# Kernel optimization log

Measured on AMD Instinct MI355X. Metric: run time of the kernel, lower is better.

Reference implementation:

```python
import jax, jax.numpy as jnp
import numpy as np

B = 8192
E = 1024  # embedding_size
P = 512   # projection_size
TEMPERATURE = 0.1
NEG_INF = -9e15
EPS = 1e-8


def setup_inputs() -> dict:
    key = jax.random.key(0)
    kx, kw, kb = jax.random.split(key, 3)
    x = jax.random.normal(kx, (B, 2 * E), dtype=jnp.float32)
    lim = 1.0 / np.sqrt(E)
    # torch nn.Linear default init: uniform(-1/sqrt(in), 1/sqrt(in))
    w = jax.random.uniform(kw, (E, P), jnp.float32, -lim, lim)
    b = jax.random.uniform(kb, (P,), jnp.float32, -lim, lim)
    return {"x": x, "w": w, "b": b}


def reference(x, w, b):
    e = x.shape[1] // 2
    # NOTE: source applies codon_projection to BOTH halves (aminoacid_projection unused)
    z_codon = jax.nn.relu(x[:, :e]) @ w + b          # [B, P]
    z_amino = jax.nn.relu(x[:, e:]) @ w + b          # [B, P]
    z = jnp.concatenate([z_codon, z_amino], axis=1)  # [B, 2P]

    # cosine similarity via normalize + GEMM instead of O(B^2*D) broadcast
    norm = jnp.maximum(jnp.linalg.norm(z, axis=-1, keepdims=True), EPS)
    zn = z / norm
    cos_sim = zn @ zn.T                              # [B, B]

    n = cos_sim.shape[0]
    idx = jnp.arange(n)
    # mask self-similarity BEFORE temperature division (matches source order)
    cos_sim = jnp.where(idx[:, None] == idx[None, :], NEG_INF, cos_sim)
    cos_sim = cos_sim / TEMPERATURE

    # pos_mask = eye rolled by B//2 along dim 0: pos[i] = cos_sim[i, (i - B//2) % B]
    pos = cos_sim[idx, (idx - n // 2) % n]
    nll = -pos + jax.nn.logsumexp(cos_sim, axis=-1)
    return nll.mean()
```

## Files before the change

kernel.cpp:

```cpp
#include <hip/hip_runtime.h>
#include <hip/hip_bf16.h>
#include <stdint.h>


typedef __attribute__((ext_vector_type(8))) __bf16 bf16x8;
typedef __attribute__((ext_vector_type(4))) float f32x4;
typedef __attribute__((ext_vector_type(4))) int i32x4;
typedef __attribute__((ext_vector_type(8))) int i32x8;

__device__ __forceinline__ unsigned short f2bf(float f) {
  union { float f; unsigned int u; } v; v.f = f;
  unsigned int u = v.u;
  u += 0x7FFFu + ((u >> 16) & 1u);
  return (unsigned short)(u >> 16);
}

__device__ __forceinline__ float bf2f(unsigned short s) {
  return __uint_as_float(((unsigned int)s) << 16);
}

__global__ __launch_bounds__(256) void prep2_kernel(
    const float* __restrict__ x, const float* __restrict__ w,
    unsigned char* __restrict__ x8, unsigned char* __restrict__ wt8,
    float* __restrict__ sumexp, float* __restrict__ out) {
  int tid = blockIdx.x * 256 + threadIdx.x;
  float4 v = ((const float4*)x)[tid];
  int p = __builtin_amdgcn_cvt_pk_fp8_f32(fmaxf(v.x, 0.f) * 16.f,
                                          fmaxf(v.y, 0.f) * 16.f, 0, false);
  p = __builtin_amdgcn_cvt_pk_fp8_f32(fmaxf(v.z, 0.f) * 16.f,
                                      fmaxf(v.w, 0.f) * 16.f, p, true);
  ((int*)x8)[tid] = p;
  if (tid < 512 * 1024) {
    int k = tid & 1023, n = tid >> 10;
    int q = __builtin_amdgcn_cvt_pk_fp8_f32(w[k * 512 + n] * 64.f, 0.f, 0, false);
    wt8[(n << 10) + k] = (unsigned char)(q & 0xFF);
  }
  if (tid < 8192) sumexp[tid] = 0.f;
  if (tid == 0) out[0] = 0.f;
}

__global__ __launch_bounds__(256) void gemm1q_kernel(
    const unsigned char* __restrict__ x8, const unsigned char* __restrict__ wt8,
    const float* __restrict__ bias, unsigned short* __restrict__ z) {
  __shared__ unsigned char As[16384] __attribute__((aligned(16)));
  __shared__ unsigned char Bs[16384] __attribute__((aligned(16)));
  int b = blockIdx.x;
  int kk = b >> 3;
  int i0 = ((b & 7) * 16 + (kk >> 2)) * 128;
  int n0 = (kk & 3) * 128;

  int tid = threadIdx.x, L = tid & 63, w = tid >> 6;
  int wm = w >> 1, wn = w & 1;
  int l4 = L & 15, q = L >> 4;
  int panel = q * 4096;

  int lp = L ^ ((L >> 3) & 7);
  int srow = w * 32 + (lp >> 1), sh = lp & 1;

  f32x4 acc[4][4];
#pragma unroll
  for (int a = 0; a < 4; ++a)
#pragma unroll
    for (int bq = 0; bq < 4; ++bq) acc[a][bq] = (f32x4)0.f;

  const unsigned char* Ag = x8 + (size_t)(i0 + srow) * 1024 + sh * 16;
  const unsigned char* Bg = wt8 + (size_t)(n0 + srow) * 1024 + sh * 16;

#pragma unroll 1
  for (int k0 = 0; k0 < 1024; k0 += 128) {
    __syncthreads();
#pragma unroll
    for (int t = 0; t < 4; ++t)
      __builtin_amdgcn_global_load_lds(
          (const __attribute__((address_space(1))) void*)(Ag + k0 + t * 32),
          (__attribute__((address_space(3))) void*)(As + t * 4096 + (tid & ~63) * 16),
          16, 0, 0);
#pragma unroll
    for (int t = 0; t < 4; ++t)
      __builtin_amdgcn_global_load_lds(
          (const __attribute__((address_space(1))) void*)(Bg + k0 + t * 32),
          (__attribute__((address_space(3))) void*)(Bs + t * 4096 + (tid & ~63) * 16),
          16, 0, 0);
    __syncthreads();
    i32x8 afr[4];
#pragma unroll
    for (int mt = 0; mt < 4; ++mt) {
      int row = wm * 64 + mt * 16 + l4;
      int p0 = (row * 2) ^ ((row >> 2) & 7);
      i32x4 lo = *(const i32x4*)(As + panel + p0 * 16);
      i32x4 hi = *(const i32x4*)(As + panel + (p0 ^ 1) * 16);
      afr[mt] = (i32x8){lo.x, lo.y, lo.z, lo.w, hi.x, hi.y, hi.z, hi.w};
    }
#pragma unroll
    for (int nt = 0; nt < 4; ++nt) {
      int row = wn * 64 + nt * 16 + l4;
      int p0 = (row * 2) ^ ((row >> 2) & 7);
      i32x4 lo = *(const i32x4*)(Bs + panel + p0 * 16);
      i32x4 hi = *(const i32x4*)(Bs + panel + (p0 ^ 1) * 16);
      i32x8 bfr = (i32x8){lo.x, lo.y, lo.z, lo.w, hi.x, hi.y, hi.z, hi.w};
#pragma unroll
      for (int mt = 0; mt < 4; ++mt)
        acc[mt][nt] = __builtin_amdgcn_mfma_scale_f32_16x16x128_f8f6f4(
            afr[mt], bfr, acc[mt][nt], 0, 0,
            0, 0x7F7F7F7F, 0, 0x7F7F7F7F);
    }
  }

  const float SC = 1.0f / 1024.0f;
#pragma unroll
  for (int nt = 0; nt < 4; ++nt) {
    int n = n0 + wn * 64 + nt * 16 + l4;
    float bn = bias[n];
#pragma unroll
    for (int mt = 0; mt < 4; ++mt) {
      int ib = i0 + wm * 64 + mt * 16 + q * 4;
#pragma unroll
      for (int r = 0; r < 4; ++r)
        z[(size_t)(ib + r) * 512 + n] = f2bf(acc[mt][nt][r] * SC + bn);
    }
  }
}

__global__ __launch_bounds__(256) void norm_kernel(
    const unsigned short* __restrict__ z, unsigned char* __restrict__ zn8) {
  int row = blockIdx.x, t = threadIdx.x;
  ushort4 u = ((const ushort4*)z)[row * 256 + t];
  float a0 = bf2f(u.x), a1 = bf2f(u.y), a2 = bf2f(u.z), a3 = bf2f(u.w);
  float ss = a0 * a0 + a1 * a1 + a2 * a2 + a3 * a3;
#pragma unroll
  for (int off = 1; off < 64; off <<= 1) ss += __shfl_xor(ss, off);
  __shared__ float red[4];
  if ((t & 63) == 0) red[t >> 6] = ss;
  __syncthreads();
  float tot = red[0] + red[1] + red[2] + red[3];
  float inv = 16.f / fmaxf(sqrtf(tot), 1e-8f);
  int p = __builtin_amdgcn_cvt_pk_fp8_f32(a0 * inv, a1 * inv, 0, false);
  p = __builtin_amdgcn_cvt_pk_fp8_f32(a2 * inv, a3 * inv, p, true);
  ((int*)zn8)[row * 256 + t] = p;
}

__global__ __launch_bounds__(256, 3) void gemm2_kernel(
    const unsigned char* __restrict__ zn8,
    float* __restrict__ sumexp, float* __restrict__ pos) {
  __shared__ unsigned char As[16384] __attribute__((aligned(16)));
  __shared__ unsigned char Bs[16384] __attribute__((aligned(16)));
  int g = (blockIdx.x & 7) * 260 + (blockIdx.x >> 3);
  int SI = 0, rem = g;
#pragma unroll 1
  for (SI = 0; SI < 8; ++SI) {
    int rowcnt = 36 + (7 - SI) * 64;
    if (rem < rowcnt) break;
    rem -= rowcnt;
  }
  int bi, bj;
  if (rem < 36) {
    int ti = 0;
    while (rem >= 8 - ti) { rem -= 8 - ti; ++ti; }
    bi = SI * 8 + ti;
    bj = bi + rem;
  } else {
    rem -= 36;
    int SJ = SI + 1 + (rem >> 6);
    int l = rem & 63;
    bi = SI * 8 + (l >> 3);
    bj = SJ * 8 + (l & 7);
  }
  bool diag = (bi == bj);
  int i0 = bi * 128, j0 = bj * 128;

  int tid = threadIdx.x, L = tid & 63, w = tid >> 6;
  int wm = w >> 1, wn = w & 1;
  int l4 = L & 15;
  int panel = (L >> 4) * 4096;

  int lp = L ^ ((L >> 3) & 7);
  int srow = w * 32 + (lp >> 1), sh = lp & 1;

  f32x4 acc[4][4];
#pragma unroll
  for (int a = 0; a < 4; ++a)
#pragma unroll
    for (int bq = 0; bq < 4; ++bq) acc[a][bq] = (f32x4)0.f;

  const unsigned char* Ag = zn8 + (i0 + srow) * 1024 + sh * 16;
  const unsigned char* Bg = zn8 + (j0 + srow) * 1024 + sh * 16;
  const unsigned char* Bsrc = diag ? (const unsigned char*)As : (const unsigned char*)Bs;

#pragma unroll 1
  for (int k0 = 0; k0 < 1024; k0 += 128) {
    __syncthreads();
#pragma unroll
    for (int t = 0; t < 4; ++t)
      __builtin_amdgcn_global_load_lds(
          (const __attribute__((address_space(1))) void*)(Ag + k0 + t * 32),
          (__attribute__((address_space(3))) void*)(As + t * 4096 + (tid & ~63) * 16),
          16, 0, 0);
    if (!diag) {
#pragma unroll
      for (int t = 0; t < 4; ++t)
        __builtin_amdgcn_global_load_lds(
            (const __attribute__((address_space(1))) void*)(Bg + k0 + t * 32),
            (__attribute__((address_space(3))) void*)(Bs + t * 4096 + (tid & ~63) * 16),
            16, 0, 0);
    }
    __syncthreads();
    i32x8 afr[4];
#pragma unroll
    for (int mt = 0; mt < 4; ++mt) {
      int row = wm * 64 + mt * 16 + l4;
      int p0 = (row * 2) ^ ((row >> 2) & 7);
      i32x4 lo = *(const i32x4*)(As + panel + p0 * 16);
      i32x4 hi = *(const i32x4*)(As + panel + (p0 ^ 1) * 16);
      afr[mt] = (i32x8){lo.x, lo.y, lo.z, lo.w, hi.x, hi.y, hi.z, hi.w};
    }
#pragma unroll
    for (int nt = 0; nt < 4; ++nt) {
      int row = wn * 64 + nt * 16 + l4;
      int p0 = (row * 2) ^ ((row >> 2) & 7);
      i32x4 lo = *(const i32x4*)(Bsrc + panel + p0 * 16);
      i32x4 hi = *(const i32x4*)(Bsrc + panel + (p0 ^ 1) * 16);
      i32x8 bfr = (i32x8){lo.x, lo.y, lo.z, lo.w, hi.x, hi.y, hi.z, hi.w};
#pragma unroll
      for (int mt = 0; mt < 4; ++mt)
        acc[mt][nt] = __builtin_amdgcn_mfma_scale_f32_16x16x128_f8f6f4(
            afr[mt], bfr, acc[mt][nt], 0, 0,
            0, 0x7F7F7F7F, 0, 0x7F7F7F7F);
    }
  }

  const float SC = 10.0f / 256.0f;
  float rs[4][4];
  float cs[4] = {0.f, 0.f, 0.f, 0.f};
#pragma unroll
  for (int mt = 0; mt < 4; ++mt)
#pragma unroll
    for (int r = 0; r < 4; ++r) rs[mt][r] = 0.f;
  int ib = i0 + wm * 64 + ((L >> 4) << 2);
  int jb = j0 + wn * 64 + l4;
#pragma unroll
  for (int mt = 0; mt < 4; ++mt)
#pragma unroll
    for (int nt = 0; nt < 4; ++nt) {
      int j = jb + nt * 16;
#pragma unroll
      for (int r = 0; r < 4; ++r) {
        int i = ib + mt * 16 + r;
        float s = acc[mt][nt][r] * SC;
        if (j == (i ^ 4096)) { pos[i] = s; pos[j] = s; }
        float e = (i == j) ? 0.f : __expf(s);
        rs[mt][r] += e;
        if (!diag) cs[nt] += e;
      }
    }
#pragma unroll
  for (int mt = 0; mt < 4; ++mt)
#pragma unroll
    for (int r = 0; r < 4; ++r) {
      float v = rs[mt][r];
      v += __shfl_xor(v, 1); v += __shfl_xor(v, 2);
      v += __shfl_xor(v, 4); v += __shfl_xor(v, 8);
      rs[mt][r] = v;
    }
  int sel = l4;
  float myv = rs[0][0];
#pragma unroll
  for (int mt = 0; mt < 4; ++mt)
#pragma unroll
    for (int r = 0; r < 4; ++r)
      if (sel == mt * 4 + r) myv = rs[mt][r];
  int rowi = i0 + wm * 64 + (sel >> 2) * 16 + ((L >> 4) << 2) + (sel & 3);
  atomicAdd(&sumexp[rowi], myv);
  if (!diag) {
#pragma unroll
    for (int nt = 0; nt < 4; ++nt) {
      float v = cs[nt];
      v += __shfl_xor(v, 16); v += __shfl_xor(v, 32);
      if ((L >> 4) == 0) atomicAdd(&sumexp[jb + nt * 16], v);
    }
  }
}

__global__ __launch_bounds__(512) void finalize_kernel(
    const float* __restrict__ sumexp, const float* __restrict__ pos,
    float* __restrict__ out) {
  int t = threadIdx.x;
  int i = blockIdx.x * 512 + t;
  float s = logf(sumexp[i]) - pos[i];
#pragma unroll
  for (int off = 1; off < 64; off <<= 1) s += __shfl_xor(s, off);
  __shared__ float red[8];
  if ((t & 63) == 0) red[t >> 6] = s;
  __syncthreads();
  if (t == 0) {
    float tot = 0.f;
    for (int k2 = 0; k2 < 8; ++k2) tot += red[k2];
    atomicAdd(out, tot * (1.0f / 8192.0f));
  }
}

extern "C" void kernel_launch(void* const* d_in, const int* in_sizes, int n_in,
                              void* d_out, int out_size, void* d_ws, size_t ws_size,
                              hipStream_t stream) {
  const float* x = (const float*)d_in[0];
  const float* w = (const float*)d_in[1];
  const float* b = (const float*)d_in[2];
  float* out = (float*)d_out;
  char* ws = (char*)d_ws;
  unsigned char* wt8 = (unsigned char*)(ws);
  unsigned char* x8  = (unsigned char*)(ws + 1048576);
  unsigned short* z  = (unsigned short*)(ws + 17825792);
  unsigned char* zn8 = (unsigned char*)(ws + 68157440);
  float* sumexp      = (float*)(ws + 84934656);
  float* pos         = (float*)(ws + 84967424);

  prep2_kernel<<<16384, 256, 0, stream>>>(x, w, x8, wt8, sumexp, out);
  gemm1q_kernel<<<512, 256, 0, stream>>>(x8, wt8, b, z);
  norm_kernel<<<8192, 256, 0, stream>>>(z, zn8);
  gemm2_kernel<<<2080, 256, 0, stream>>>(zn8, sumexp, pos);
  finalize_kernel<<<16, 512, 0, stream>>>(sumexp, pos, out);
}
```

Before: 175.4 us.

## Double-buffer LDS tiles in both FP8 GEMM kernels to overlap loads with MFMA

Both GEMM kernels now use a 64 KB shared buffer split into two stages for A and B. The next K-slice is issued with global_load_lds while the current slice is consumed by MFMAs, and there is one barrier per stage instead of two. The aim is to hide global-to-LDS latency behind compute. Doubling LDS cuts gemm2 occupancy from 3 to 2 blocks per CU via launch bounds, and overlap depends on the async load not being waited on early.

```diff
diff --git a/kernel.cpp b/kernel.cpp
--- a/kernel.cpp
+++ b/kernel.cpp
@@ -39,11 +39,10 @@
   if (tid == 0) out[0] = 0.f;
 }
 
-__global__ __launch_bounds__(256) void gemm1q_kernel(
+__global__ __launch_bounds__(256, 2) void gemm1q_kernel(
     const unsigned char* __restrict__ x8, const unsigned char* __restrict__ wt8,
     const float* __restrict__ bias, unsigned short* __restrict__ z) {
-  __shared__ unsigned char As[16384] __attribute__((aligned(16)));
-  __shared__ unsigned char Bs[16384] __attribute__((aligned(16)));
+  __shared__ unsigned char smem[65536] __attribute__((aligned(16)));
   int b = blockIdx.x;
   int kk = b >> 3;
   int i0 = ((b & 7) * 16 + (kk >> 2)) * 128;
@@ -56,6 +55,7 @@
 
   int lp = L ^ ((L >> 3) & 7);
   int srow = w * 32 + (lp >> 1), sh = lp & 1;
+  int ldst = (tid & ~63) * 16;
 
   f32x4 acc[4][4];
 #pragma unroll
@@ -66,37 +66,39 @@
   const unsigned char* Ag = x8 + (size_t)(i0 + srow) * 1024 + sh * 16;
   const unsigned char* Bg = wt8 + (size_t)(n0 + srow) * 1024 + sh * 16;
 
-#pragma unroll 1
-  for (int k0 = 0; k0 < 1024; k0 += 128) {
-    __syncthreads();
+  auto stage = [&](int buf, int k0) {
 #pragma unroll
     for (int t = 0; t < 4; ++t)
       __builtin_amdgcn_global_load_lds(
           (const __attribute__((address_space(1))) void*)(Ag + k0 + t * 32),
-          (__attribute__((address_space(3))) void*)(As + t * 4096 + (tid & ~63) * 16),
+          (__attribute__((address_space(3))) void*)(smem + buf * 16384 + t * 4096 + ldst),
           16, 0, 0);
 #pragma unroll
     for (int t = 0; t < 4; ++t)
       __builtin_amdgcn_global_load_lds(
           (const __attribute__((address_space(1))) void*)(Bg + k0 + t * 32),
-          (__attribute__((address_space(3))) void*)(Bs + t * 4096 + (tid & ~63) * 16),
+          (__attribute__((address_space(3))) void*)(smem + 32768 + buf * 16384 + t * 4096 + ldst),
           16, 0, 0);
-    __syncthreads();
+  };
+
+  auto compute = [&](int buf) {
+    const unsigned char* Asb = smem + buf * 16384;
+    const unsigned char* Bsb = smem + 32768 + buf * 16384;
     i32x8 afr[4];
 #pragma unroll
     for (int mt = 0; mt < 4; ++mt) {
       int row = wm * 64 + mt * 16 + l4;
       int p0 = (row * 2) ^ ((row >> 2) & 7);
-      i32x4 lo = *(const i32x4*)(As + panel + p0 * 16);
-      i32x4 hi = *(const i32x4*)(As + panel + (p0 ^ 1) * 16);
+      i32x4 lo = *(const i32x4*)(Asb + panel + p0 * 16);
+      i32x4 hi = *(const i32x4*)(Asb + panel + (p0 ^ 1) * 16);
       afr[mt] = (i32x8){lo.x, lo.y, lo.z, lo.w, hi.x, hi.y, hi.z, hi.w};
     }
 #pragma unroll
     for (int nt = 0; nt < 4; ++nt) {
       int row = wn * 64 + nt * 16 + l4;
       int p0 = (row * 2) ^ ((row >> 2) & 7);
-      i32x4 lo = *(const i32x4*)(Bs + panel + p0 * 16);
-      i32x4 hi = *(const i32x4*)(Bs + panel + (p0 ^ 1) * 16);
+      i32x4 lo = *(const i32x4*)(Bsb + panel + p0 * 16);
+      i32x4 hi = *(const i32x4*)(Bsb + panel + (p0 ^ 1) * 16);
       i32x8 bfr = (i32x8){lo.x, lo.y, lo.z, lo.w, hi.x, hi.y, hi.z, hi.w};
 #pragma unroll
       for (int mt = 0; mt < 4; ++mt)
@@ -104,6 +106,18 @@
             afr[mt], bfr, acc[mt][nt], 0, 0,
             0, 0x7F7F7F7F, 0, 0x7F7F7F7F);
     }
+  };
+
+  stage(0, 0);
+  __syncthreads();
+#pragma unroll 1
+  for (int k0 = 0; k0 < 1024; k0 += 256) {
+    stage(1, k0 + 128);
+    compute(0);
+    __syncthreads();
+    if (k0 < 768) stage(0, k0 + 256);
+    compute(1);
+    __syncthreads();
   }
 
   const float SC = 1.0f / 1024.0f;
@@ -139,11 +153,10 @@
   ((int*)zn8)[row * 256 + t] = p;
 }
 
-__global__ __launch_bounds__(256, 3) void gemm2_kernel(
+__global__ __launch_bounds__(256, 2) void gemm2_kernel(
     const unsigned char* __restrict__ zn8,
     float* __restrict__ sumexp, float* __restrict__ pos) {
-  __shared__ unsigned char As[16384] __attribute__((aligned(16)));
-  __shared__ unsigned char Bs[16384] __attribute__((aligned(16)));
+  __shared__ unsigned char smem[65536] __attribute__((aligned(16)));
   int g = (blockIdx.x & 7) * 260 + (blockIdx.x >> 3);
   int SI = 0, rem = g;
 #pragma unroll 1
@@ -175,6 +188,7 @@
 
   int lp = L ^ ((L >> 3) & 7);
   int srow = w * 32 + (lp >> 1), sh = lp & 1;
+  int ldst = (tid & ~63) * 16;
 
   f32x4 acc[4][4];
 #pragma unroll
@@ -184,41 +198,42 @@
 
   const unsigned char* Ag = zn8 + (i0 + srow) * 1024 + sh * 16;
   const unsigned char* Bg = zn8 + (j0 + srow) * 1024 + sh * 16;
-  const unsigned char* Bsrc = diag ? (const unsigned char*)As : (const unsigned char*)Bs;
-
-#pragma unroll 1
-  for (int k0 = 0; k0 < 1024; k0 += 128) {
-    __syncthreads();
+
+  auto stageA = [&](int buf, int k0) {
 #pragma unroll
     for (int t = 0; t < 4; ++t)
       __builtin_amdgcn_global_load_lds(
           (const __attribute__((address_space(1))) void*)(Ag + k0 + t * 32),
-          (__attribute__((address_space(3))) void*)(As + t * 4096 + (tid & ~63) * 16),
+          (__attribute__((address_space(3))) void*)(smem + buf * 16384 + t * 4096 + ldst),
           16, 0, 0);
-    if (!diag) {
-#pragma unroll
-      for (int t = 0; t < 4; ++t)
-        __builtin_amdgcn_global_load_lds(
-            (const __attribute__((address_space(1))) void*)(Bg + k0 + t * 32),
-            (__attribute__((address_space(3))) void*)(Bs + t * 4096 + (tid & ~63) * 16),
-            16, 0, 0);
-    }
-    __syncthreads();
+  };
+  auto stageB = [&](int buf, int k0) {
+#pragma unroll
+    for (int t = 0; t < 4; ++t)
+      __builtin_amdgcn_global_load_lds(
+          (const __attribute__((address_space(1))) void*)(Bg + k0 + t * 32),
+          (__attribute__((address_space(3))) void*)(smem + 32768 + buf * 16384 + t * 4096 + ldst),
+          16, 0, 0);
+  };
+
+  auto compute = [&](int buf) {
+    const unsigned char* Asb = smem + buf * 16384;
+    const unsigned char* Bsb = diag ? Asb : smem + 32768 + buf * 16384;
     i32x8 afr[4];
 #pragma unroll
     for (int mt = 0; mt < 4; ++mt) {
       int row = wm * 64 + mt * 16 + l4;
       int p0 = (row * 2) ^ ((row >> 2) & 7);
-      i32x4 lo = *(const i32x4*)(As + panel + p0 * 16);
-      i32x4 hi = *(const i32x4*)(As + panel + (p0 ^ 1) * 16);
+      i32x4 lo = *(const i32x4*)(Asb + panel + p0 * 16);
+      i32x4 hi = *(const i32x4*)(Asb + panel + (p0 ^ 1) * 16);
       afr[mt] = (i32x8){lo.x, lo.y, lo.z, lo.w, hi.x, hi.y, hi.z, hi.w};
     }
 #pragma unroll
     for (int nt = 0; nt < 4; ++nt) {
       int row = wn * 64 + nt * 16 + l4;
       int p0 = (row * 2) ^ ((row >> 2) & 7);
-      i32x4 lo = *(const i32x4*)(Bsrc + panel + p0 * 16);
-      i32x4 hi = *(const i32x4*)(Bsrc + panel + (p0 ^ 1) * 16);
+      i32x4 lo = *(const i32x4*)(Bsb + panel + p0 * 16);
+      i32x4 hi = *(const i32x4*)(Bsb + panel + (p0 ^ 1) * 16);
       i32x8 bfr = (i32x8){lo.x, lo.y, lo.z, lo.w, hi.x, hi.y, hi.z, hi.w};
 #pragma unroll
       for (int mt = 0; mt < 4; ++mt)
@@ -226,6 +241,23 @@
             afr[mt], bfr, acc[mt][nt], 0, 0,
             0, 0x7F7F7F7F, 0, 0x7F7F7F7F);
     }
+  };
+
+  stageA(0, 0);
+  if (!diag) stageB(0, 0);
+  __syncthreads();
+#pragma unroll 1
+  for (int k0 = 0; k0 < 1024; k0 += 256) {
+    stageA(1, k0 + 128);
+    if (!diag) stageB(1, k0 + 128);
+    compute(0);
+    __syncthreads();
+    if (k0 < 768) {
+      stageA(0, k0 + 256);
+      if (!diag) stageB(0, k0 + 256);
+    }
+    compute(1);
+    __syncthreads();
   }
 
   const float SC = 10.0f / 256.0f;
```

New measurement: 176.5 us. About the same (+0.6%).

## Enlarge gram GEMM tiles to 256x256 with double-buffered LDS and interleaved prefetch

Applied to the files above, without the earlier changes.

Reworks the symmetric fp8 gram GEMM from 128x128 tiles with 4 waves to 256x256 tiles with 8 waves over 528 upper-triangle blocks. K-chunks go into double-buffered 128KB LDS, and the next chunk's global-to-LDS loads are split into quarters interleaved between MFMA phases, with setprio and barriers in between. The aim is more operand reuse per byte loaded and hiding load latency behind compute. The cost is one block per CU because of the large LDS, many more barriers, and fewer blocks, which may leave load imbalance across CUs.

```diff
diff --git a/kernel.cpp b/kernel.cpp
--- a/kernel.cpp
+++ b/kernel.cpp
@@ -3,7 +3,6 @@
 #include <stdint.h>
 
 
-typedef __attribute__((ext_vector_type(8))) __bf16 bf16x8;
 typedef __attribute__((ext_vector_type(4))) float f32x4;
 typedef __attribute__((ext_vector_type(4))) int i32x4;
 typedef __attribute__((ext_vector_type(8))) int i32x8;
@@ -139,106 +138,169 @@
   ((int*)zn8)[row * 256 + t] = p;
 }
 
-__global__ __launch_bounds__(256, 3) void gemm2_kernel(
+__global__ __launch_bounds__(512) void gemm2_kernel(
     const unsigned char* __restrict__ zn8,
     float* __restrict__ sumexp, float* __restrict__ pos) {
-  __shared__ unsigned char As[16384] __attribute__((aligned(16)));
-  __shared__ unsigned char Bs[16384] __attribute__((aligned(16)));
-  int g = (blockIdx.x & 7) * 260 + (blockIdx.x >> 3);
-  int SI = 0, rem = g;
+  __shared__ unsigned char smem[131072] __attribute__((aligned(16)));
+  int g = (blockIdx.x & 7) * 66 + (blockIdx.x >> 3);
+  int rem = g, bi = 0;
 #pragma unroll 1
-  for (SI = 0; SI < 8; ++SI) {
-    int rowcnt = 36 + (7 - SI) * 64;
-    if (rem < rowcnt) break;
-    rem -= rowcnt;
-  }
-  int bi, bj;
-  if (rem < 36) {
-    int ti = 0;
-    while (rem >= 8 - ti) { rem -= 8 - ti; ++ti; }
-    bi = SI * 8 + ti;
-    bj = bi + rem;
-  } else {
-    rem -= 36;
-    int SJ = SI + 1 + (rem >> 6);
-    int l = rem & 63;
-    bi = SI * 8 + (l >> 3);
-    bj = SJ * 8 + (l & 7);
-  }
+  while (rem >= 32 - bi) { rem -= 32 - bi; ++bi; }
+  int bj = bi + rem;
   bool diag = (bi == bj);
-  int i0 = bi * 128, j0 = bj * 128;
+  int i0 = bi * 256, j0 = bj * 256;
 
   int tid = threadIdx.x, L = tid & 63, w = tid >> 6;
-  int wm = w >> 1, wn = w & 1;
-  int l4 = L & 15;
-  int panel = (L >> 4) * 4096;
+  int wm = w >> 2, wn = w & 3;
+  int l4 = L & 15, q = L >> 4;
+  int panel = q * 8192;
 
   int lp = L ^ ((L >> 3) & 7);
   int srow = w * 32 + (lp >> 1), sh = lp & 1;
-
-  f32x4 acc[4][4];
-#pragma unroll
-  for (int a = 0; a < 4; ++a)
+  int ldst = (tid & ~63) * 16;
+
+  int pA[8], pB[4];
+#pragma unroll
+  for (int mt = 0; mt < 8; ++mt) {
+    int r = wm * 128 + mt * 16 + l4;
+    pA[mt] = ((r * 2) ^ ((r >> 2) & 7)) * 16;
+  }
+#pragma unroll
+  for (int nt = 0; nt < 4; ++nt) {
+    int r = wn * 64 + nt * 16 + l4;
+    pB[nt] = ((r * 2) ^ ((r >> 2) & 7)) * 16;
+  }
+
+  f32x4 acc[8][4];
+#pragma unroll
+  for (int a = 0; a < 8; ++a)
 #pragma unroll
     for (int bq = 0; bq < 4; ++bq) acc[a][bq] = (f32x4)0.f;
 
-  const unsigned char* Ag = zn8 + (i0 + srow) * 1024 + sh * 16;
-  const unsigned char* Bg = zn8 + (j0 + srow) * 1024 + sh * 16;
-  const unsigned char* Bsrc = diag ? (const unsigned char*)As : (const unsigned char*)Bs;
+  const unsigned char* Ag = zn8 + (size_t)(i0 + srow) * 1024 + sh * 16;
+  const unsigned char* Bg = zn8 + (size_t)(j0 + srow) * 1024 + sh * 16;
+
+  auto stA = [&](int nc, int kk, int t) {
+    __builtin_amdgcn_global_load_lds(
+        (const __attribute__((address_space(1))) void*)(Ag + kk + t * 32),
+        (__attribute__((address_space(3))) void*)(smem + nc * 32768 + t * 8192 + ldst),
+        16, 0, 0);
+  };
+  auto stB = [&](int nc, int kk, int t) {
+    __builtin_amdgcn_global_load_lds(
+        (const __attribute__((address_space(1))) void*)(Bg + kk + t * 32),
+        (__attribute__((address_space(3))) void*)(smem + 65536 + nc * 32768 + t * 8192 + ldst),
+        16, 0, 0);
+  };
+
+  stA(0, 0, 0); stA(0, 0, 1); stA(0, 0, 2); stA(0, 0, 3);
+  if (!diag) { stB(0, 0, 0); stB(0, 0, 1); stB(0, 0, 2); stB(0, 0, 3); }
+  asm volatile("s_waitcnt vmcnt(0)" ::: "memory");
+  __builtin_amdgcn_s_barrier();
+  __builtin_amdgcn_sched_barrier(0);
 
 #pragma unroll 1
-  for (int k0 = 0; k0 < 1024; k0 += 128) {
-    __syncthreads();
-#pragma unroll
-    for (int t = 0; t < 4; ++t)
-      __builtin_amdgcn_global_load_lds(
-          (const __attribute__((address_space(1))) void*)(Ag + k0 + t * 32),
-          (__attribute__((address_space(3))) void*)(As + t * 4096 + (tid & ~63) * 16),
-          16, 0, 0);
-    if (!diag) {
-#pragma unroll
-      for (int t = 0; t < 4; ++t)
-        __builtin_amdgcn_global_load_lds(
-            (const __attribute__((address_space(1))) void*)(Bg + k0 + t * 32),
-            (__attribute__((address_space(3))) void*)(Bs + t * 4096 + (tid & ~63) * 16),
-            16, 0, 0);
-    }
-    __syncthreads();
-    i32x8 afr[4];
+  for (int t = 0; t < 8; ++t) {
+    int c = t & 1, nc = c ^ 1;
+    const unsigned char* Asb = smem + c * 32768;
+    const unsigned char* Bsb = diag ? Asb : smem + 65536 + c * 32768;
+    int k1 = t * 128 + 128;
+    bool st = (t < 7);
+
+    i32x8 afr[4], bf0[2], bf1[2];
 #pragma unroll
     for (int mt = 0; mt < 4; ++mt) {
-      int row = wm * 64 + mt * 16 + l4;
-      int p0 = (row * 2) ^ ((row >> 2) & 7);
-      i32x4 lo = *(const i32x4*)(As + panel + p0 * 16);
-      i32x4 hi = *(const i32x4*)(As + panel + (p0 ^ 1) * 16);
+      i32x4 lo = *(const i32x4*)(Asb + panel + pA[mt]);
+      i32x4 hi = *(const i32x4*)(Asb + panel + (pA[mt] ^ 16));
       afr[mt] = (i32x8){lo.x, lo.y, lo.z, lo.w, hi.x, hi.y, hi.z, hi.w};
     }
 #pragma unroll
-    for (int nt = 0; nt < 4; ++nt) {
-      int row = wn * 64 + nt * 16 + l4;
-      int p0 = (row * 2) ^ ((row >> 2) & 7);
-      i32x4 lo = *(const i32x4*)(Bsrc + panel + p0 * 16);
-      i32x4 hi = *(const i32x4*)(Bsrc + panel + (p0 ^ 1) * 16);
-      i32x8 bfr = (i32x8){lo.x, lo.y, lo.z, lo.w, hi.x, hi.y, hi.z, hi.w};
-#pragma unroll
-      for (int mt = 0; mt < 4; ++mt)
+    for (int nt = 0; nt < 2; ++nt) {
+      i32x4 lo = *(const i32x4*)(Bsb + panel + pB[nt]);
+      i32x4 hi = *(const i32x4*)(Bsb + panel + (pB[nt] ^ 16));
+      bf0[nt] = (i32x8){lo.x, lo.y, lo.z, lo.w, hi.x, hi.y, hi.z, hi.w};
+    }
+    if (st) { stA(nc, k1, 0); stA(nc, k1, 1); }
+    __builtin_amdgcn_s_barrier();
+    __builtin_amdgcn_sched_barrier(0);
+    __builtin_amdgcn_s_setprio(1);
+#pragma unroll
+    for (int mt = 0; mt < 4; ++mt)
+#pragma unroll
+      for (int nt = 0; nt < 2; ++nt)
         acc[mt][nt] = __builtin_amdgcn_mfma_scale_f32_16x16x128_f8f6f4(
-            afr[mt], bfr, acc[mt][nt], 0, 0,
-            0, 0x7F7F7F7F, 0, 0x7F7F7F7F);
-    }
+            afr[mt], bf0[nt], acc[mt][nt], 0, 0, 0, 0x7F7F7F7F, 0, 0x7F7F7F7F);
+    __builtin_amdgcn_s_setprio(0);
+    __builtin_amdgcn_s_barrier();
+    __builtin_amdgcn_sched_barrier(0);
+
+#pragma unroll
+    for (int nt = 0; nt < 2; ++nt) {
+      i32x4 lo = *(const i32x4*)(Bsb + panel + pB[2 + nt]);
+      i32x4 hi = *(const i32x4*)(Bsb + panel + (pB[2 + nt] ^ 16));
+      bf1[nt] = (i32x8){lo.x, lo.y, lo.z, lo.w, hi.x, hi.y, hi.z, hi.w};
+    }
+    if (st) { stA(nc, k1, 2); stA(nc, k1, 3); }
+    __builtin_amdgcn_s_barrier();
+    __builtin_amdgcn_sched_barrier(0);
+    __builtin_amdgcn_s_setprio(1);
+#pragma unroll
+    for (int mt = 0; mt < 4; ++mt)
+#pragma unroll
+      for (int nt = 0; nt < 2; ++nt)
+        acc[mt][2 + nt] = __builtin_amdgcn_mfma_scale_f32_16x16x128_f8f6f4(
+            afr[mt], bf1[nt], acc[mt][2 + nt], 0, 0, 0, 0x7F7F7F7F, 0, 0x7F7F7F7F);
+    __builtin_amdgcn_s_setprio(0);
+    __builtin_amdgcn_s_barrier();
+    __builtin_amdgcn_sched_barrier(0);
+
+#pragma unroll
+    for (int mt = 0; mt < 4; ++mt) {
+      i32x4 lo = *(const i32x4*)(Asb + panel + pA[4 + mt]);
+      i32x4 hi = *(const i32x4*)(Asb + panel + (pA[4 + mt] ^ 16));
+      afr[mt] = (i32x8){lo.x, lo.y, lo.z, lo.w, hi.x, hi.y, hi.z, hi.w};
+    }
+    if (st && !diag) { stB(nc, k1, 0); stB(nc, k1, 1); }
+    __builtin_amdgcn_s_barrier();
+    __builtin_amdgcn_sched_barrier(0);
+    __builtin_amdgcn_s_setprio(1);
+#pragma unroll
+    for (int mt = 0; mt < 4; ++mt)
+#pragma unroll
+      for (int nt = 0; nt < 2; ++nt)
+        acc[4 + mt][2 + nt] = __builtin_amdgcn_mfma_scale_f32_16x16x128_f8f6f4(
+            afr[mt], bf1[nt], acc[4 + mt][2 + nt], 0, 0, 0, 0x7F7F7F7F, 0, 0x7F7F7F7F);
+    __builtin_amdgcn_s_setprio(0);
+    __builtin_amdgcn_s_barrier();
+    __builtin_amdgcn_sched_barrier(0);
+
+    if (st && !diag) { stB(nc, k1, 2); stB(nc, k1, 3); }
+    __builtin_amdgcn_s_barrier();
+    __builtin_amdgcn_sched_barrier(0);
+    __builtin_amdgcn_s_setprio(1);
+#pragma unroll
+    for (int mt = 0; mt < 4; ++mt)
+#pragma unroll
+      for (int nt = 0; nt < 2; ++nt)
+        acc[4 + mt][nt] = __builtin_amdgcn_mfma_scale_f32_16x16x128_f8f6f4(
+            afr[mt], bf0[nt], acc[4 + mt][nt], 0, 0, 0, 0x7F7F7F7F, 0, 0x7F7F7F7F);
+    __builtin_amdgcn_s_setprio(0);
+    asm volatile("s_waitcnt vmcnt(0)" ::: "memory");
+    __builtin_amdgcn_s_barrier();
+    __builtin_amdgcn_sched_barrier(0);
   }
 
   const float SC = 10.0f / 256.0f;
-  float rs[4][4];
+  float rs[8][4];
   float cs[4] = {0.f, 0.f, 0.f, 0.f};
 #pragma unroll
-  for (int mt = 0; mt < 4; ++mt)
+  for (int mt = 0; mt < 8; ++mt)
 #pragma unroll
     for (int r = 0; r < 4; ++r) rs[mt][r] = 0.f;
-  int ib = i0 + wm * 64 + ((L >> 4) << 2);
+  int ib = i0 + wm * 128 + q * 4;
   int jb = j0 + wn * 64 + l4;
 #pragma unroll
-  for (int mt = 0; mt < 4; ++mt)
+  for (int mt = 0; mt < 8; ++mt)
 #pragma unroll
     for (int nt = 0; nt < 4; ++nt) {
       int j = jb + nt * 16;
@@ -253,7 +315,7 @@
       }
     }
 #pragma unroll
-  for (int mt = 0; mt < 4; ++mt)
+  for (int mt = 0; mt < 8; ++mt)
 #pragma unroll
     for (int r = 0; r < 4; ++r) {
       float v = rs[mt][r];
@@ -261,21 +323,22 @@
       v += __shfl_xor(v, 4); v += __shfl_xor(v, 8);
       rs[mt][r] = v;
     }
-  int sel = l4;
-  float myv = rs[0][0];
+  float v1 = rs[0][0], v2 = rs[4][0];
 #pragma unroll
   for (int mt = 0; mt < 4; ++mt)
 #pragma unroll
-    for (int r = 0; r < 4; ++r)
-      if (sel == mt * 4 + r) myv = rs[mt][r];
-  int rowi = i0 + wm * 64 + (sel >> 2) * 16 + ((L >> 4) << 2) + (sel & 3);
-  atomicAdd(&sumexp[rowi], myv);
+    for (int r = 0; r < 4; ++r) {
+      if (l4 == mt * 4 + r) { v1 = rs[mt][r]; v2 = rs[4 + mt][r]; }
+    }
+  int rowi = ib + (l4 >> 2) * 16 + (l4 & 3);
+  atomicAdd(&sumexp[rowi], v1);
+  atomicAdd(&sumexp[rowi + 64], v2);
   if (!diag) {
 #pragma unroll
     for (int nt = 0; nt < 4; ++nt) {
       float v = cs[nt];
       v += __shfl_xor(v, 16); v += __shfl_xor(v, 32);
-      if ((L >> 4) == 0) atomicAdd(&sumexp[jb + nt * 16], v);
+      if (q == 0) atomicAdd(&sumexp[jb + nt * 16], v);
     }
   }
 }
@@ -316,6 +379,6 @@
   prep2_kernel<<<16384, 256, 0, stream>>>(x, w, x8, wt8, sumexp, out);
   gemm1q_kernel<<<512, 256, 0, stream>>>(x8, wt8, b, z);
   norm_kernel<<<8192, 256, 0, stream>>>(z, zn8);
-  gemm2_kernel<<<2080, 256, 0, stream>>>(zn8, sumexp, pos);
+  gemm2_kernel<<<528, 512, 0, stream>>>(zn8, sumexp, pos);
   finalize_kernel<<<16, 512, 0, stream>>>(sumexp, pos, out);
 }
```

New measurement: 194.7 us. +11.0%, slower.

## Use two waves per 128x128 tile with 128x64 warp tiles in gemm2

Applied to the files above, without the earlier changes.

The similarity GEMM block drops from four waves (each a 64x64 subtile) to two waves, each covering a 128x64 subtile with 8x4 MFMA accumulators. This gives more MFMAs per LDS fragment load and precomputes the swizzled LDS offsets once. Each thread now issues twice as many global-to-LDS loads and does two row atomics. The cost is much higher register use (128 accumulator floats per thread), fewer waves per CU and less latency hiding.

```diff
diff --git a/kernel.cpp b/kernel.cpp
--- a/kernel.cpp
+++ b/kernel.cpp
@@ -3,7 +3,6 @@
 #include <stdint.h>
 
 
-typedef __attribute__((ext_vector_type(8))) __bf16 bf16x8;
 typedef __attribute__((ext_vector_type(4))) float f32x4;
 typedef __attribute__((ext_vector_type(4))) int i32x4;
 typedef __attribute__((ext_vector_type(8))) int i32x8;
@@ -139,7 +138,7 @@
   ((int*)zn8)[row * 256 + t] = p;
 }
 
-__global__ __launch_bounds__(256, 3) void gemm2_kernel(
+__global__ __launch_bounds__(128, 2) void gemm2_kernel(
     const unsigned char* __restrict__ zn8,
     float* __restrict__ sumexp, float* __restrict__ pos) {
   __shared__ unsigned char As[16384] __attribute__((aligned(16)));
@@ -169,76 +168,96 @@
   int i0 = bi * 128, j0 = bj * 128;
 
   int tid = threadIdx.x, L = tid & 63, w = tid >> 6;
-  int wm = w >> 1, wn = w & 1;
-  int l4 = L & 15;
-  int panel = (L >> 4) * 4096;
-
-  int lp = L ^ ((L >> 3) & 7);
-  int srow = w * 32 + (lp >> 1), sh = lp & 1;
-
-  f32x4 acc[4][4];
-#pragma unroll
-  for (int a = 0; a < 4; ++a)
+  int l4 = L & 15, q = L >> 4;
+  int panel = q * 4096;
+  int lw = w * 1024;
+
+  int e = tid ^ ((tid >> 3) & 7);
+  int r2 = e >> 1, hh = e & 1;
+
+  int pA[8], pB[4];
+#pragma unroll
+  for (int mt = 0; mt < 8; ++mt) {
+    int r = mt * 16 + l4;
+    pA[mt] = ((r * 2) ^ ((r >> 2) & 7)) * 16;
+  }
+#pragma unroll
+  for (int nt = 0; nt < 4; ++nt) {
+    int r = w * 64 + nt * 16 + l4;
+    pB[nt] = ((r * 2) ^ ((r >> 2) & 7)) * 16;
+  }
+
+  f32x4 acc[8][4];
+#pragma unroll
+  for (int a = 0; a < 8; ++a)
 #pragma unroll
     for (int bq = 0; bq < 4; ++bq) acc[a][bq] = (f32x4)0.f;
 
-  const unsigned char* Ag = zn8 + (i0 + srow) * 1024 + sh * 16;
-  const unsigned char* Bg = zn8 + (j0 + srow) * 1024 + sh * 16;
+  const unsigned char* Ag0 = zn8 + (size_t)(i0 + r2) * 1024 + hh * 16;
+  const unsigned char* Ag1 = zn8 + (size_t)(i0 + 64 + r2) * 1024 + hh * 16;
+  const unsigned char* Bg0 = zn8 + (size_t)(j0 + r2) * 1024 + hh * 16;
+  const unsigned char* Bg1 = zn8 + (size_t)(j0 + 64 + r2) * 1024 + hh * 16;
   const unsigned char* Bsrc = diag ? (const unsigned char*)As : (const unsigned char*)Bs;
 
 #pragma unroll 1
   for (int k0 = 0; k0 < 1024; k0 += 128) {
     __syncthreads();
 #pragma unroll
-    for (int t = 0; t < 4; ++t)
+    for (int p = 0; p < 4; ++p) {
       __builtin_amdgcn_global_load_lds(
-          (const __attribute__((address_space(1))) void*)(Ag + k0 + t * 32),
-          (__attribute__((address_space(3))) void*)(As + t * 4096 + (tid & ~63) * 16),
+          (const __attribute__((address_space(1))) void*)(Ag0 + k0 + p * 32),
+          (__attribute__((address_space(3))) void*)(As + p * 4096 + lw),
           16, 0, 0);
+      __builtin_amdgcn_global_load_lds(
+          (const __attribute__((address_space(1))) void*)(Ag1 + k0 + p * 32),
+          (__attribute__((address_space(3))) void*)(As + p * 4096 + 2048 + lw),
+          16, 0, 0);
+    }
     if (!diag) {
 #pragma unroll
-      for (int t = 0; t < 4; ++t)
+      for (int p = 0; p < 4; ++p) {
         __builtin_amdgcn_global_load_lds(
-            (const __attribute__((address_space(1))) void*)(Bg + k0 + t * 32),
-            (__attribute__((address_space(3))) void*)(Bs + t * 4096 + (tid & ~63) * 16),
+            (const __attribute__((address_space(1))) void*)(Bg0 + k0 + p * 32),
+            (__attribute__((address_space(3))) void*)(Bs + p * 4096 + lw),
             16, 0, 0);
+        __builtin_amdgcn_global_load_lds(
+            (const __attribute__((address_space(1))) void*)(Bg1 + k0 + p * 32),
+            (__attribute__((address_space(3))) void*)(Bs + p * 4096 + 2048 + lw),
+            16, 0, 0);
+      }
     }
     __syncthreads();
-    i32x8 afr[4];
-#pragma unroll
-    for (int mt = 0; mt < 4; ++mt) {
-      int row = wm * 64 + mt * 16 + l4;
-      int p0 = (row * 2) ^ ((row >> 2) & 7);
-      i32x4 lo = *(const i32x4*)(As + panel + p0 * 16);
-      i32x4 hi = *(const i32x4*)(As + panel + (p0 ^ 1) * 16);
-      afr[mt] = (i32x8){lo.x, lo.y, lo.z, lo.w, hi.x, hi.y, hi.z, hi.w};
-    }
+    i32x8 bfr[4];
 #pragma unroll
     for (int nt = 0; nt < 4; ++nt) {
-      int row = wn * 64 + nt * 16 + l4;
-      int p0 = (row * 2) ^ ((row >> 2) & 7);
-      i32x4 lo = *(const i32x4*)(Bsrc + panel + p0 * 16);
-      i32x4 hi = *(const i32x4*)(Bsrc + panel + (p0 ^ 1) * 16);
-      i32x8 bfr = (i32x8){lo.x, lo.y, lo.z, lo.w, hi.x, hi.y, hi.z, hi.w};
-#pragma unroll
-      for (int mt = 0; mt < 4; ++mt)
+      i32x4 lo = *(const i32x4*)(Bsrc + panel + pB[nt]);
+      i32x4 hi = *(const i32x4*)(Bsrc + panel + (pB[nt] ^ 16));
+      bfr[nt] = (i32x8){lo.x, lo.y, lo.z, lo.w, hi.x, hi.y, hi.z, hi.w};
+    }
+#pragma unroll
+    for (int mt = 0; mt < 8; ++mt) {
+      i32x4 lo = *(const i32x4*)(As + panel + pA[mt]);
+      i32x4 hi = *(const i32x4*)(As + panel + (pA[mt] ^ 16));
+      i32x8 afr = (i32x8){lo.x, lo.y, lo.z, lo.w, hi.x, hi.y, hi.z, hi.w};
+#pragma unroll
+      for (int nt = 0; nt < 4; ++nt)
         acc[mt][nt] = __builtin_amdgcn_mfma_scale_f32_16x16x128_f8f6f4(
-            afr[mt], bfr, acc[mt][nt], 0, 0,
+            afr, bfr[nt], acc[mt][nt], 0, 0,
             0, 0x7F7F7F7F, 0, 0x7F7F7F7F);
     }
   }
 
   const float SC = 10.0f / 256.0f;
-  float rs[4][4];
+  float rs[8][4];
   float cs[4] = {0.f, 0.f, 0.f, 0.f};
 #pragma unroll
-  for (int mt = 0; mt < 4; ++mt)
+  for (int mt = 0; mt < 8; ++mt)
 #pragma unroll
     for (int r = 0; r < 4; ++r) rs[mt][r] = 0.f;
-  int ib = i0 + wm * 64 + ((L >> 4) << 2);
-  int jb = j0 + wn * 64 + l4;
-#pragma unroll
-  for (int mt = 0; mt < 4; ++mt)
+  int ib = i0 + q * 4;
+  int jb = j0 + w * 64 + l4;
+#pragma unroll
+  for (int mt = 0; mt < 8; ++mt)
 #pragma unroll
     for (int nt = 0; nt < 4; ++nt) {
       int j = jb + nt * 16;
@@ -247,13 +266,13 @@
         int i = ib + mt * 16 + r;
         float s = acc[mt][nt][r] * SC;
         if (j == (i ^ 4096)) { pos[i] = s; pos[j] = s; }
-        float e = (i == j) ? 0.f : __expf(s);
-        rs[mt][r] += e;
-        if (!diag) cs[nt] += e;
+        float e2 = (i == j) ? 0.f : __expf(s);
+        rs[mt][r] += e2;
+        if (!diag) cs[nt] += e2;
       }
     }
 #pragma unroll
-  for (int mt = 0; mt < 4; ++mt)
+  for (int mt = 0; mt < 8; ++mt)
 #pragma unroll
     for (int r = 0; r < 4; ++r) {
       float v = rs[mt][r];
@@ -261,21 +280,22 @@
       v += __shfl_xor(v, 4); v += __shfl_xor(v, 8);
       rs[mt][r] = v;
     }
-  int sel = l4;
-  float myv = rs[0][0];
+  float v1 = rs[0][0], v2 = rs[4][0];
 #pragma unroll
   for (int mt = 0; mt < 4; ++mt)
 #pragma unroll
-    for (int r = 0; r < 4; ++r)
-      if (sel == mt * 4 + r) myv = rs[mt][r];
-  int rowi = i0 + wm * 64 + (sel >> 2) * 16 + ((L >> 4) << 2) + (sel & 3);
-  atomicAdd(&sumexp[rowi], myv);
+    for (int r = 0; r < 4; ++r) {
+      if (l4 == mt * 4 + r) { v1 = rs[mt][r]; v2 = rs[4 + mt][r]; }
+    }
+  int rowi = ib + (l4 >> 2) * 16 + (l4 & 3);
+  atomicAdd(&sumexp[rowi], v1);
+  atomicAdd(&sumexp[rowi + 64], v2);
   if (!diag) {
 #pragma unroll
     for (int nt = 0; nt < 4; ++nt) {
       float v = cs[nt];
       v += __shfl_xor(v, 16); v += __shfl_xor(v, 32);
-      if ((L >> 4) == 0) atomicAdd(&sumexp[jb + nt * 16], v);
+      if (q == 0) atomicAdd(&sumexp[jb + nt * 16], v);
     }
   }
 }
@@ -316,6 +336,6 @@
   prep2_kernel<<<16384, 256, 0, stream>>>(x, w, x8, wt8, sumexp, out);
   gemm1q_kernel<<<512, 256, 0, stream>>>(x8, wt8, b, z);
   norm_kernel<<<8192, 256, 0, stream>>>(z, zn8);
-  gemm2_kernel<<<2080, 256, 0, stream>>>(zn8, sumexp, pos);
+  gemm2_kernel<<<2080, 128, 0, stream>>>(zn8, sumexp, pos);
   finalize_kernel<<<16, 512, 0, stream>>>(sumexp, pos, out);
 }
```

After: 183.3 us. 4.5% more time.
